# Optimization experiments

Measured on AMD Instinct MI355X. Metric: run time of the kernel, lower is better.

Reference implementation:

```python
import jax, jax.numpy as jnp
import numpy as np

K = 20        # kNN neighborhood size (args.k)
EPS = 1e-5    # BatchNorm eps
SLOPE = 0.2   # LeakyReLU negative slope
B, N = 8, 2048


def lrelu(x):
    return jnp.where(x >= 0, x, SLOPE * x)


def bn_cn(x):  # BatchNorm1d over [B, C, N] (training-mode batch stats, gamma=1, beta=0)
    m = jnp.mean(x, axis=(0, 2), keepdims=True)
    v = jnp.var(x, axis=(0, 2), keepdims=True)
    return (x - m) * jax.lax.rsqrt(v + EPS)


def bn_f(x):  # BatchNorm1d over [B, F]
    m = jnp.mean(x, axis=0, keepdims=True)
    v = jnp.var(x, axis=0, keepdims=True)
    return (x - m) * jax.lax.rsqrt(v + EPS)


def conv_bn(x, w):  # 1x1 Conv1d (no bias) + BN + LeakyReLU; x [B,C,N], w [O,C]
    return lrelu(bn_cn(jnp.einsum('oc,bcn->bon', w, x)))


def knn_idx(x, k):  # x [B,C,N] -> [B,N,k] nearest neighbors, self excluded
    sq = jnp.sum(x * x, axis=1)                                   # [B,N]
    pd = 2.0 * jnp.einsum('bcn,bcm->bnm', x, x) - sq[:, :, None] - sq[:, None, :]
    return jax.lax.top_k(pd, k + 1)[1][:, :, 1:]                  # drop self (max = 0)


def self_att(x, wq, wk, wv, wc):  # SelfAttention block (n_heads=1, scale_dot)
    idx = knn_idx(x, K)                                           # [B,N,K]
    feats = jnp.swapaxes(x, 1, 2)                                 # [B,N,C]
    nb = jax.vmap(lambda f, i: f[i])(feats, idx)                  # [B,N,K,C] gather
    E = wq.shape[0]
    q = feats @ wq.T                                              # [B,N,E]
    kk = nb @ wk.T                                                # [B,N,K,E]
    v = (nb - feats[:, :, None, :]) @ wv.T                        # [B,N,K,V]
    scores = jax.nn.softmax(jnp.einsum('bne,bnke->bnk', q, kk) / np.float32(np.sqrt(E)), axis=-1)
    out = jnp.einsum('bnk,bnkv->bnv', scores, v)                  # [B,N,V]
    res = conv_bn(jnp.swapaxes(out, 1, 2), wc)                    # [B,O,N]
    return jnp.concatenate([res, x], axis=1)


def setup_inputs() -> dict:
    key = jax.random.key(0)
    ks = jax.random.split(key, 32)
    w = lambda k, o, i: jax.random.normal(k, (o, i), jnp.float32) / np.float32(np.sqrt(i))
    d = {'x': jax.random.normal(ks[0], (B, 3, N), jnp.float32)}
    dims = {1: 3, 2: 64, 3: 64, 4: 128}
    j = 1
    for s, c in dims.items():
        for nm in ('wq', 'wk', 'wv', 'wc'):
            d[f'sa{s}_{nm}'] = w(ks[j], c, c); j += 1
    d['conv1_w'] = w(ks[17], 64, 6)
    d['conv2_w'] = w(ks[18], 64, 128)
    d['conv3_w'] = w(ks[19], 128, 128)
    d['conv4_w'] = w(ks[20], 256, 256)
    d['conv5_w'] = w(ks[21], 1024, 512)
    d['lin1_w'] = w(ks[22], 512, 2048); d['lin1_b'] = jnp.zeros((512,), jnp.float32)
    d['lin2_w'] = w(ks[23], 256, 512);  d['lin2_b'] = jnp.zeros((256,), jnp.float32)
    d['lin3_w'] = w(ks[24], 40, 256);   d['lin3_b'] = jnp.zeros((40,), jnp.float32)
    return d


def reference(x, sa1_wq, sa1_wk, sa1_wv, sa1_wc, sa2_wq, sa2_wk, sa2_wv, sa2_wc,
              sa3_wq, sa3_wk, sa3_wv, sa3_wc, sa4_wq, sa4_wk, sa4_wv, sa4_wc,
              conv1_w, conv2_w, conv3_w, conv4_w, conv5_w,
              lin1_w, lin1_b, lin2_w, lin2_b, lin3_w, lin3_b):
    h = self_att(x, sa1_wq, sa1_wk, sa1_wv, sa1_wc)        # [B,6,N]
    x1 = conv_bn(h, conv1_w)                               # [B,64,N]
    h = self_att(x1, sa2_wq, sa2_wk, sa2_wv, sa2_wc)       # [B,128,N]
    x2 = conv_bn(h, conv2_w)                               # [B,64,N]
    h = self_att(x2, sa3_wq, sa3_wk, sa3_wv, sa3_wc)       # [B,128,N]
    x3 = conv_bn(h, conv3_w)                               # [B,128,N]
    h = self_att(x3, sa4_wq, sa4_wk, sa4_wv, sa4_wc)       # [B,256,N]
    x4 = conv_bn(h, conv4_w)                               # [B,256,N]
    xc = jnp.concatenate([x1, x2, x3, x4], axis=1)         # [B,512,N]
    x5 = conv_bn(xc, conv5_w)                              # [B,1024,N]
    p = jnp.concatenate([jnp.max(x5, axis=2), jnp.mean(x5, axis=2)], axis=1)  # [B,2048]
    h = lrelu(bn_f(p @ lin1_w.T + lin1_b))                 # dropout = identity (eval)
    h = lrelu(bn_f(h @ lin2_w.T + lin2_b))
    return h @ lin3_w.T + lin3_b                           # [B,40]
```

## Files before the change

kernel.cpp:

```cpp
#include <hip/hip_runtime.h>
#include <math.h>

#define BB 8
#define NN 2048
#define KNB 20

typedef __attribute__((ext_vector_type(8))) short bf16x8;
typedef __attribute__((ext_vector_type(8))) _Float16 f16x8;
typedef __attribute__((ext_vector_type(4))) float f32x4;

__device__ inline unsigned short f2bf(float f) {
  union { float f; unsigned u; } v; v.f = f;
  unsigned r = v.u + 0x7FFF + ((v.u >> 16) & 1);
  return (unsigned short)(r >> 16);
}

__device__ inline float lrelu(float v) { return v >= 0.f ? v : 0.2f * v; }

template <bool F16SPLIT, bool BF16>
__global__ __launch_bounds__(256) void xprep_kernel(
    const float* __restrict__ in, int inBS, int C,
    float* __restrict__ xT, _Float16* __restrict__ hi, _Float16* __restrict__ lo,
    unsigned short* __restrict__ bf, float* __restrict__ sq) {
  __shared__ float tile[32][33];
  __shared__ float ps[8][33];
  int b = blockIdx.z;
  const float* ip = in + (size_t)b * inBS;
  int c0 = blockIdx.x * 32;
  int r0 = blockIdx.y * 32;
  int tx = threadIdx.x & 31, ty = threadIdx.x >> 5;
  float s = 0.f;
  for (int yy = ty; yy < 32; yy += 8) {
    int r = r0 + yy;
    float v = (r < C) ? ip[(size_t)r * NN + c0 + tx] : 0.f;
    tile[yy][tx] = v;
    s += v * v;
  }
  ps[ty][tx] = s;
  __syncthreads();
  if (ty == 0) {
    float a = ps[0][tx];
#pragma unroll
    for (int u = 1; u < 8; ++u) a += ps[u][tx];
    atomicAdd(&sq[b * NN + c0 + tx], a);
  }
  for (int yy = ty; yy < 32; yy += 8) {
    int c = c0 + yy, r = r0 + tx;
    if (r < C) {
      float v = tile[tx][yy];
      size_t o = (size_t)b * NN * C + (size_t)c * C + r;
      xT[o] = v;
      if (F16SPLIT) {
        _Float16 hv = (_Float16)v;
        hi[o] = hv;
        lo[o] = (_Float16)(v - (float)hv);
      }
      if (BF16) bf[o] = f2bf(v);
    }
  }
}

__global__ __launch_bounds__(256) void xprep3_kernel(const float* __restrict__ in,
                                                     float* __restrict__ xT,
                                                     float* __restrict__ xs4) {
  int b = blockIdx.z;
  int n = blockIdx.x * 256 + threadIdx.x;
  const float* ip = in + (size_t)b * 3 * NN;
  float x0 = ip[n], x1 = ip[NN + n], x2 = ip[2 * NN + n];
  float s = x0 * x0 + x1 * x1 + x2 * x2;
  size_t o = (size_t)b * NN + n;
  xT[o * 3 + 0] = x0; xT[o * 3 + 1] = x1; xT[o * 3 + 2] = x2;
  *(float4*)&xs4[o * 4] = make_float4(x0, x1, x2, s);
}

__global__ __launch_bounds__(256) void prep_mw_kernel(
    const float* __restrict__ wq, const float* __restrict__ wk,
    const float* __restrict__ wv, const float* __restrict__ wc, int C,
    float* __restrict__ M, float* __restrict__ WCV,
    unsigned short* __restrict__ Mb, unsigned short* __restrict__ wcvb, int emitBF) {
  int w = blockIdx.x * 4 + (threadIdx.x >> 6);
  int lane = threadIdx.x & 63;
  int total = 2 * C * C;
  if (w >= total) return;
  float a = 0.f;
  if (w < C * C) {
    int c = w / C, cp = w - c * C;
    for (int e = lane; e < C; e += 64) a += wk[e * C + c] * wq[e * C + cp];
  } else {
    int t = w - C * C;
    int o = t / C, c = t - o * C;
    for (int e = lane; e < C; e += 64) a += wc[o * C + e] * wv[e * C + c];
  }
#pragma unroll
  for (int s = 32; s > 0; s >>= 1) a += __shfl_down(a, s);
  if (lane == 0) {
    if (w < C * C) {
      M[w] = a;
      if (emitBF) Mb[w] = f2bf(a);
    } else {
      int t = w - C * C;
      WCV[t] = a;
      if (emitBF) wcvb[t] = f2bf(a);
    }
  }
}

__global__ __launch_bounds__(256) void convert_bf16_kernel(const float* __restrict__ in,
                                                           unsigned short* __restrict__ out,
                                                           int count) {
  int i = blockIdx.x * 256 + threadIdx.x;
  if (i < count) out[i] = f2bf(in[i]);
}

__global__ __launch_bounds__(256) void transpose_kernel(const float* __restrict__ in, int inBS,
                                                        int R, int Cl, float* __restrict__ out) {
  __shared__ float tile[32][33];
  int b = blockIdx.z;
  const float* ip = in + (size_t)b * inBS;
  float* op = out + (size_t)b * R * Cl;
  int c0 = blockIdx.x * 32, r0 = blockIdx.y * 32;
  int tx = threadIdx.x & 31, ty = threadIdx.x >> 5;
  for (int yy = ty; yy < 32; yy += 8) {
    int r = r0 + yy, c = c0 + tx;
    tile[yy][tx] = (r < R && c < Cl) ? ip[(size_t)r * Cl + c] : 0.f;
  }
  __syncthreads();
  for (int yy = ty; yy < 32; yy += 8) {
    int c = c0 + yy, r = r0 + tx;
    if (c < Cl && r < R) op[(size_t)c * R + r] = tile[tx][yy];
  }
}

__global__ __launch_bounds__(256) void transpose_bf16_kernel(const float* __restrict__ in, int inBS,
                                                             int R, int Cl,
                                                             unsigned short* __restrict__ out) {
  __shared__ float tile[32][33];
  int b = blockIdx.z;
  const float* ip = in + (size_t)b * inBS;
  unsigned short* op = out + (size_t)b * R * Cl;
  int c0 = blockIdx.x * 32, r0 = blockIdx.y * 32;
  int tx = threadIdx.x & 31, ty = threadIdx.x >> 5;
  for (int yy = ty; yy < 32; yy += 8) {
    int r = r0 + yy, c = c0 + tx;
    tile[yy][tx] = (r < R && c < Cl) ? ip[(size_t)r * Cl + c] : 0.f;
  }
  __syncthreads();
  for (int yy = ty; yy < 32; yy += 8) {
    int c = c0 + yy, r = r0 + tx;
    if (c < Cl && r < R) op[(size_t)c * R + r] = f2bf(tile[tx][yy]);
  }
}

template <bool TOUT>
__global__ __launch_bounds__(256, 2) void mfma_gemm_lds_kernel(
    const unsigned short* __restrict__ A, const unsigned short* __restrict__ B,
    float* __restrict__ Z, int O, int K) {
  const int b = blockIdx.z;
  const int n0 = blockIdx.x * 128, o0 = blockIdx.y * 128;
  const int tid = threadIdx.x;
  const int wave = tid >> 6, lane = tid & 63;
  const int wo = wave >> 1, wn = wave & 1;
  const int l16 = lane & 15, q = lane >> 4;
  __shared__ unsigned short Al[2][4096];
  __shared__ unsigned short Bl[2][4096];
  const unsigned short* Ab = A + (size_t)o0 * K;
  const unsigned short* Bb = B + ((size_t)b * NN + n0) * K;

  const int p0 = tid, p1 = tid + 256;
  const int r0 = ((p0 >> 6) << 4) | (p0 & 15), c0 = ((p0 >> 4) & 3) * 8;
  const int r1 = ((p1 >> 6) << 4) | (p1 & 15), c1 = ((p1 >> 4) & 3) * 8;

  bf16x8 ar0, ar1, br0, br1;
  auto gload = [&](int k0) {
    ar0 = *(const bf16x8*)(Ab + (size_t)r0 * K + k0 + c0);
    ar1 = *(const bf16x8*)(Ab + (size_t)r1 * K + k0 + c1);
    br0 = *(const bf16x8*)(Bb + (size_t)r0 * K + k0 + c0);
    br1 = *(const bf16x8*)(Bb + (size_t)r1 * K + k0 + c1);
  };
  auto sstore = [&](int buf) {
    *(bf16x8*)&Al[buf][p0 * 8] = ar0;
    *(bf16x8*)&Al[buf][p1 * 8] = ar1;
    *(bf16x8*)&Bl[buf][p0 * 8] = br0;
    *(bf16x8*)&Bl[buf][p1 * 8] = br1;
  };

  f32x4 acc[4][4];
#pragma unroll
  for (int s = 0; s < 4; ++s)
#pragma unroll
    for (int t = 0; t < 4; ++t) acc[s][t] = (f32x4){0.f, 0.f, 0.f, 0.f};

  gload(0);
  sstore(0);
  int cur = 0;
  for (int k0 = 0; k0 < K; k0 += 32) {
    bool more = (k0 + 32) < K;
    if (more) gload(k0 + 32);
    __syncthreads();
    bf16x8 af[4], bfr[4];
#pragma unroll
    for (int s = 0; s < 4; ++s)
      af[s] = *(const bf16x8*)&Al[cur][((wo * 4 + s) * 64 + q * 16 + l16) * 8];
#pragma unroll
    for (int t = 0; t < 4; ++t)
      bfr[t] = *(const bf16x8*)&Bl[cur][((wn * 4 + t) * 64 + q * 16 + l16) * 8];
#pragma unroll
    for (int s = 0; s < 4; ++s)
#pragma unroll
      for (int t = 0; t < 4; ++t)
        acc[s][t] = __builtin_amdgcn_mfma_f32_16x16x32_bf16(af[s], bfr[t], acc[s][t], 0, 0, 0);
    if (more) sstore(cur ^ 1);
    cur ^= 1;
  }
#pragma unroll
  for (int s = 0; s < 4; ++s)
#pragma unroll
    for (int t = 0; t < 4; ++t) {
      if (TOUT) {
        int n = n0 + wn * 64 + t * 16 + l16;
        int ob = o0 + wo * 64 + s * 16 + q * 4;
        *(f32x4*)&Z[((size_t)b * NN + n) * O + ob] = acc[s][t];
      } else {
        float* zp = Z + ((size_t)b * O + o0 + wo * 64 + s * 16 + q * 4) * NN
                    + n0 + wn * 64 + t * 16 + l16;
#pragma unroll
        for (int r = 0; r < 4; ++r) zp[(size_t)r * NN] = acc[s][t][r];
      }
    }
}

__global__ __launch_bounds__(256, 2) void pd_mfma_kernel(
    const _Float16* __restrict__ xhi, const _Float16* __restrict__ xlo, int C,
    const float* __restrict__ sq, float* __restrict__ P, int b_base) {
  const int bl = blockIdx.z;
  const int b = b_base + bl;
  const int n0 = blockIdx.x * 128, m0 = blockIdx.y * 128;
  const int tid = threadIdx.x;
  const int wave = tid >> 6, lane = tid & 63;
  const int wn_ = wave >> 1, wm_ = wave & 1;
  const int l16 = lane & 15, q = lane >> 4;
  __shared__ _Float16 Ah[4096], Al[4096], Bh[4096], Bl[4096];
  const _Float16* Ahg = xhi + ((size_t)b * NN + n0) * C;
  const _Float16* Alg = xlo + ((size_t)b * NN + n0) * C;
  const _Float16* Bhg = xhi + ((size_t)b * NN + m0) * C;
  const _Float16* Blg = xlo + ((size_t)b * NN + m0) * C;

  const int p0 = tid, p1 = tid + 256;
  const int r0 = ((p0 >> 6) << 4) | (p0 & 15), c0 = ((p0 >> 4) & 3) * 8;
  const int r1 = ((p1 >> 6) << 4) | (p1 & 15), c1 = ((p1 >> 4) & 3) * 8;

  f32x4 acc[4][4];
#pragma unroll
  for (int s = 0; s < 4; ++s)
#pragma unroll
    for (int t = 0; t < 4; ++t) acc[s][t] = (f32x4){0.f, 0.f, 0.f, 0.f};

  for (int k0 = 0; k0 < C; k0 += 32) {
    __syncthreads();
    *(f16x8*)&Ah[p0 * 8] = *(const f16x8*)(Ahg + (size_t)r0 * C + k0 + c0);
    *(f16x8*)&Ah[p1 * 8] = *(const f16x8*)(Ahg + (size_t)r1 * C + k0 + c1);
    *(f16x8*)&Al[p0 * 8] = *(const f16x8*)(Alg + (size_t)r0 * C + k0 + c0);
    *(f16x8*)&Al[p1 * 8] = *(const f16x8*)(Alg + (size_t)r1 * C + k0 + c1);
    *(f16x8*)&Bh[p0 * 8] = *(const f16x8*)(Bhg + (size_t)r0 * C + k0 + c0);
    *(f16x8*)&Bh[p1 * 8] = *(const f16x8*)(Bhg + (size_t)r1 * C + k0 + c1);
    *(f16x8*)&Bl[p0 * 8] = *(const f16x8*)(Blg + (size_t)r0 * C + k0 + c0);
    *(f16x8*)&Bl[p1 * 8] = *(const f16x8*)(Blg + (size_t)r1 * C + k0 + c1);
    __syncthreads();
    f16x8 ah[4], al[4], bh[4], blv[4];
#pragma unroll
    for (int s = 0; s < 4; ++s) {
      int pi = ((wn_ * 4 + s) * 64 + q * 16 + l16) * 8;
      ah[s] = *(const f16x8*)&Ah[pi];
      al[s] = *(const f16x8*)&Al[pi];
    }
#pragma unroll
    for (int t = 0; t < 4; ++t) {
      int pi = ((wm_ * 4 + t) * 64 + q * 16 + l16) * 8;
      bh[t] = *(const f16x8*)&Bh[pi];
      blv[t] = *(const f16x8*)&Bl[pi];
    }
#pragma unroll
    for (int s = 0; s < 4; ++s)
#pragma unroll
      for (int t = 0; t < 4; ++t) {
        acc[s][t] = __builtin_amdgcn_mfma_f32_16x16x32_f16(ah[s], bh[t], acc[s][t], 0, 0, 0);
        acc[s][t] = __builtin_amdgcn_mfma_f32_16x16x32_f16(ah[s], blv[t], acc[s][t], 0, 0, 0);
        acc[s][t] = __builtin_amdgcn_mfma_f32_16x16x32_f16(al[s], bh[t], acc[s][t], 0, 0, 0);
      }
  }
#pragma unroll
  for (int s = 0; s < 4; ++s)
#pragma unroll
    for (int t = 0; t < 4; ++t) {
      int col = m0 + wm_ * 64 + t * 16 + l16;
      float sqv = sq[b * NN + col];
      float* pp = P + ((size_t)bl * NN + n0 + wn_ * 64 + s * 16 + q * 4) * NN + col;
#pragma unroll
      for (int r = 0; r < 4; ++r) pp[(size_t)r * NN] = 2.f * acc[s][t][r] - sqv;
    }
}

__global__ __launch_bounds__(256) void topk_bsort_kernel(const float* __restrict__ P,
                                                         int* __restrict__ idx_out, int b_base) {
  const int wave = threadIdx.x >> 6;
  const int lane = threadIdx.x & 63;
  const int n = blockIdx.x * 4 + wave;
  const int bl = blockIdx.y;
  const int b = b_base + bl;
  const float4* rp = (const float4*)(P + ((size_t)bl * NN + n) * NN);
  unsigned key[32];
#pragma unroll
  for (int q = 0; q < 8; ++q) {
    float4 vv = rp[q * 64 + lane];
    int mb = q * 256 + lane * 4;
    float fv[4] = {vv.x, vv.y, vv.z, vv.w};
#pragma unroll
    for (int j = 0; j < 4; ++j) {
      unsigned u = __float_as_uint(fv[j]);
      unsigned mask = (unsigned)(((int)u) >> 31) | 0x80000000u;
      unsigned sl = (unsigned)(q * 4 + j);
      key[q * 4 + j] = (mb + j == n) ? sl : (((u ^ mask) & 0xFFFFFFE0u) | sl);
    }
  }
#pragma unroll
  for (int k = 2; k <= 32; k <<= 1) {
#pragma unroll
    for (int j = k >> 1; j > 0; j >>= 1) {
#pragma unroll
      for (int i = 0; i < 32; ++i) {
        int l = i ^ j;
        if (l > i) {
          unsigned ka = key[i], kb = key[l];
          unsigned mx = ka > kb ? ka : kb;
          unsigned mn = ka > kb ? kb : ka;
          if ((i & k) == 0) { key[i] = mx; key[l] = mn; }
          else              { key[i] = mn; key[l] = mx; }
        }
      }
    }
  }
  int* op = idx_out + (size_t)(b * NN + n) * KNB;
  for (int k = 0; k < KNB; ++k) {
    unsigned best = key[0];
#pragma unroll
    for (int s = 32; s > 0; s >>= 1) {
      unsigned o = (unsigned)__shfl_xor((int)best, s);
      best = best > o ? best : o;
    }
    unsigned long long bal = __ballot(key[0] == best);
    if (lane == (int)__ffsll(bal) - 1) {
      unsigned sl = key[0] & 31u;
      op[k] = (int)((sl >> 2) * 256u + (unsigned)lane * 4u + (sl & 3u));
#pragma unroll
      for (int j = 0; j < 20; ++j) key[j] = key[j + 1];
    }
  }
}

__global__ __launch_bounds__(256) void topk_c3_kernel(const float* __restrict__ xs4,
                                                      int* __restrict__ idx_out) {
  const int wave = threadIdx.x >> 6;
  const int lane = threadIdx.x & 63;
  const int n = blockIdx.x * 4 + wave;
  const int b = blockIdx.y;
  const float4* xp = (const float4*)(xs4 + (size_t)b * NN * 4);
  float4 me = xp[n];
  float tx = 2.f * me.x, ty = 2.f * me.y, tz = 2.f * me.z;
  unsigned key[32];
#pragma unroll
  for (int s = 0; s < 32; ++s) {
    int m = s * 64 + lane;
    float4 c = xp[m];
    float pd = tx * c.x + ty * c.y + tz * c.z - c.w;
    unsigned u = __float_as_uint(pd);
    unsigned mask = (unsigned)(((int)u) >> 31) | 0x80000000u;
    key[s] = (m == n) ? (unsigned)s : ((((u ^ mask) & 0xFFFFFFE0u)) | (unsigned)s);
  }
#pragma unroll
  for (int k = 2; k <= 32; k <<= 1) {
#pragma unroll
    for (int j = k >> 1; j > 0; j >>= 1) {
#pragma unroll
// ... 207 lines not shown
#pragma unroll
    for (int s = 32; s > 0; s >>= 1) p[k] += __shfl_xor(p[k], s);
  }
  const float scale = (C == 128) ? 0.088388347648318447f : 0.125f;
  float mx = p[0];
#pragma unroll
  for (int k = 1; k < KNB; ++k) mx = fmaxf(mx, p[k]);
  float sum = 0.f;
#pragma unroll
  for (int k = 0; k < KNB; ++k) {
    p[k] = expf((p[k] - mx) * scale);
    sum += p[k];
  }
  float inv = 1.f / sum;
  float a0 = 0.f, a1 = 0.f;
#pragma unroll
  for (int k = 0; k < KNB; ++k) {
    a0 += p[k] * v0[k];
    if (C == 128) a1 += p[k] * v1[k];
  }
  float r0 = a0 * inv - xTb[(size_t)n * C + lane];
  float r1;
  if (C == 128) r1 = a1 * inv - xTb[(size_t)n * C + 64 + lane];
  if (BF16OUT) {
    AGGtb[(size_t)gid * C + lane] = f2bf(r0);
    if (C == 128) AGGtb[(size_t)gid * C + 64 + lane] = f2bf(r1);
  } else {
    AGGt[(size_t)gid * C + lane] = r0;
    if (C == 128) AGGt[(size_t)gid * C + 64 + lane] = r1;
  }
}

template <int C, bool BF16OUT>
__global__ __launch_bounds__(64) void att_wave_kernel(
    const float* __restrict__ xT, const float* __restrict__ UT,
    const int* __restrict__ idx, float* __restrict__ AGGt,
    unsigned short* __restrict__ AGGtb) {
  const int n = blockIdx.x & (NN - 1);
  const int b = blockIdx.x >> 11;
  const int lane = threadIdx.x;
  constexpr int CP = C + 1;
  __shared__ float nb[KNB][CP];
  __shared__ float sl[KNB];
  __shared__ int nidx[KNB];
  __shared__ float ul[C];
  const float* xTb = xT + (size_t)b * NN * C;
  if (lane < KNB) nidx[lane] = idx[(size_t)(b * NN + n) * KNB + lane] & (NN - 1);
  for (int c = lane; c < C; c += 64) ul[c] = UT[((size_t)b * NN + n) * C + c];
  __syncthreads();
  for (int i = lane; i < KNB * C; i += 64) {
    int k = i / C, c = i - k * C;
    nb[k][c] = xTb[(size_t)nidx[k] * C + c];
  }
  __syncthreads();
  float sv = -INFINITY;
  if (lane < KNB) {
    float a = 0.f;
#pragma unroll
    for (int c = 0; c < C; ++c) a += nb[lane][c] * ul[c];
    sv = a / sqrtf((float)C);
  }
  float mx = sv;
#pragma unroll
  for (int s = 32; s > 0; s >>= 1) mx = fmaxf(mx, __shfl_xor(mx, s));
  float e = (lane < KNB) ? expf(sv - mx) : 0.f;
  float sum = e;
#pragma unroll
  for (int s = 32; s > 0; s >>= 1) sum += __shfl_xor(sum, s);
  if (lane < KNB) sl[lane] = e / sum;
  __syncthreads();
  const float* xTn = xTb + (size_t)n * C;
  for (int c = lane; c < C; c += 64) {
    float a = 0.f;
#pragma unroll
    for (int k = 0; k < KNB; ++k) a += sl[k] * nb[k][c];
    float r = a - xTn[c];
    if (BF16OUT)
      AGGtb[((size_t)b * NN + n) * C + c] = f2bf(r);
    else
      AGGt[((size_t)b * NN + n) * C + c] = r;
  }
}

__global__ __launch_bounds__(256) void bn_fused_kernel(const float* __restrict__ z, int O,
                                                       float* __restrict__ out, int outBS, int c0) {
  int o = blockIdx.x;
  int tid = threadIdx.x;
  __shared__ float s1[256], s2[256];
  __shared__ float smv, srv;
  float a1 = 0.f, a2 = 0.f;
  for (int i = tid; i < BB * 512; i += 256) {
    int b = i >> 9, n4 = i & 511;
    float4 v = *(const float4*)&z[((size_t)b * O + o) * NN + n4 * 4];
    a1 += v.x + v.y + v.z + v.w;
    a2 += v.x * v.x + v.y * v.y + v.z * v.z + v.w * v.w;
  }
  s1[tid] = a1; s2[tid] = a2;
  __syncthreads();
  for (int st = 128; st > 0; st >>= 1) {
    if (tid < st) { s1[tid] += s1[tid + st]; s2[tid] += s2[tid + st]; }
    __syncthreads();
  }
  if (tid == 0) {
    float m = s1[0] / (BB * NN);
    float var = s2[0] / (BB * NN) - m * m;
    smv = m; srv = rsqrtf(var + 1e-5f);
  }
  __syncthreads();
  float m = smv, r = srv;
  for (int i = tid; i < BB * 512; i += 256) {
    int b = i >> 9, n4 = i & 511;
    float4 v = *(const float4*)&z[((size_t)b * O + o) * NN + n4 * 4];
    float4 ov;
    ov.x = lrelu((v.x - m) * r); ov.y = lrelu((v.y - m) * r);
    ov.z = lrelu((v.z - m) * r); ov.w = lrelu((v.w - m) * r);
    *(float4*)&out[(size_t)b * outBS + (size_t)(c0 + o) * NN + n4 * 4] = ov;
  }
}

__global__ __launch_bounds__(256) void bn_copy_kernel(const float* __restrict__ z, int O,
                                                      const float* __restrict__ xin, int xbs,
                                                      float* __restrict__ out) {
  int o = blockIdx.x;
  int tid = threadIdx.x;
  int outBS = 2 * O * NN;
  if (o >= O) {
    int c = o - O;
    for (int i = tid; i < BB * 512; i += 256) {
      int b = i >> 9, n4 = i & 511;
      *(float4*)&out[(size_t)b * outBS + (size_t)o * NN + n4 * 4] =
          *(const float4*)&xin[(size_t)b * xbs + (size_t)c * NN + n4 * 4];
    }
    return;
  }
  __shared__ float s1[256], s2[256];
  __shared__ float smv, srv;
  float a1 = 0.f, a2 = 0.f;
  for (int i = tid; i < BB * 512; i += 256) {
    int b = i >> 9, n4 = i & 511;
    float4 v = *(const float4*)&z[((size_t)b * O + o) * NN + n4 * 4];
    a1 += v.x + v.y + v.z + v.w;
    a2 += v.x * v.x + v.y * v.y + v.z * v.z + v.w * v.w;
  }
  s1[tid] = a1; s2[tid] = a2;
  __syncthreads();
  for (int st = 128; st > 0; st >>= 1) {
    if (tid < st) { s1[tid] += s1[tid + st]; s2[tid] += s2[tid + st]; }
    __syncthreads();
  }
  if (tid == 0) {
    float m = s1[0] / (BB * NN);
    float var = s2[0] / (BB * NN) - m * m;
    smv = m; srv = rsqrtf(var + 1e-5f);
  }
  __syncthreads();
  float m = smv, r = srv;
  for (int i = tid; i < BB * 512; i += 256) {
    int b = i >> 9, n4 = i & 511;
    float4 v = *(const float4*)&z[((size_t)b * O + o) * NN + n4 * 4];
    float4 ov;
    ov.x = lrelu((v.x - m) * r); ov.y = lrelu((v.y - m) * r);
    ov.z = lrelu((v.z - m) * r); ov.w = lrelu((v.w - m) * r);
    *(float4*)&out[(size_t)b * outBS + (size_t)o * NN + n4 * 4] = ov;
  }
}

__global__ __launch_bounds__(256) void bn_pool_kernel(const float* __restrict__ z,
                                                      float* __restrict__ p) {
  int o = blockIdx.x;
  int tid = threadIdx.x;
  __shared__ float s1[256], s2[256];
  __shared__ float smv, srv;
  float a1 = 0.f, a2 = 0.f;
  for (int i = tid; i < BB * 512; i += 256) {
    int b = i >> 9, n4 = i & 511;
    float4 v = *(const float4*)&z[((size_t)b * 1024 + o) * NN + n4 * 4];
    a1 += v.x + v.y + v.z + v.w;
    a2 += v.x * v.x + v.y * v.y + v.z * v.z + v.w * v.w;
  }
  s1[tid] = a1; s2[tid] = a2;
  __syncthreads();
  for (int st = 128; st > 0; st >>= 1) {
    if (tid < st) { s1[tid] += s1[tid + st]; s2[tid] += s2[tid + st]; }
    __syncthreads();
  }
  if (tid == 0) {
    float m = s1[0] / (BB * NN);
    float var = s2[0] / (BB * NN) - m * m;
    smv = m; srv = rsqrtf(var + 1e-5f);
  }
  __syncthreads();
  float m = smv, r = srv;
  int b = tid >> 5, l = tid & 31;
  const float* zp = z + ((size_t)b * 1024 + o) * NN;
  float mx = -INFINITY, sm = 0.f;
  for (int j = l; j < 512; j += 32) {
    float4 v = *(const float4*)&zp[j * 4];
    float vx = lrelu((v.x - m) * r), vy = lrelu((v.y - m) * r);
    float vz = lrelu((v.z - m) * r), vw = lrelu((v.w - m) * r);
    mx = fmaxf(mx, fmaxf(fmaxf(vx, vy), fmaxf(vz, vw)));
    sm += vx + vy + vz + vw;
  }
#pragma unroll
  for (int s = 16; s > 0; s >>= 1) {
    mx = fmaxf(mx, __shfl_xor(mx, s));
    sm += __shfl_xor(sm, s);
  }
  if (l == 0) {
    p[b * 2048 + o] = mx;
    p[b * 2048 + 1024 + o] = sm * (1.f / NN);
  }
}

__global__ __launch_bounds__(64) void linear_kernel(const float* __restrict__ in, int IN, int OUT,
                                                    const float* __restrict__ w,
                                                    const float* __restrict__ bias,
                                                    float* __restrict__ out) {
  int o = blockIdx.x;
  int b = o / OUT, f = o % OUT;
  const float* ip = in + (size_t)b * IN;
  const float* wp = w + (size_t)f * IN;
  float a = 0.f;
  for (int i = threadIdx.x; i < IN; i += 64) a += ip[i] * wp[i];
#pragma unroll
  for (int s = 32; s > 0; s >>= 1) a += __shfl_down(a, s);
  if (threadIdx.x == 0) out[o] = a + bias[f];
}

__global__ __launch_bounds__(256) void bnf_kernel(float* __restrict__ t, int F) {
  int f = blockIdx.x * blockDim.x + threadIdx.x;
  if (f >= F) return;
  float s = 0.f, s2 = 0.f;
  for (int b = 0; b < BB; ++b) { float v = t[b * F + f]; s += v; s2 += v * v; }
  float m = s * (1.f / BB);
  float var = s2 * (1.f / BB) - m * m;
  float r = rsqrtf(var + 1e-5f);
  for (int b = 0; b < BB; ++b) {
    float v = (t[b * F + f] - m) * r;
    t[b * F + f] = v >= 0.f ? v : 0.2f * v;
  }
}


struct SAW { const float *wq, *wk, *wv, *wc; };

static inline void run_conv(const float* in, int inBS, int C, int O, const float* w,
                            float* z, hipStream_t st) {
  if (O % 128 == 0)
    conv_gemm128_db_kernel<<<dim3(NN / 128, O / 128, BB), 256, 0, st>>>(in, inBS, C, O, w, z);
  else
    conv_gemm_kernel<false, false><<<dim3(NN / 64, (O + 63) / 64, BB), 256, 0, st>>>(in, inBS, C, O, w, z);
}

template <int C, bool MFMA>
static inline void run_sa(const float* xin, int xbs, SAW w,
                          float* xT, float* UT, float* AGGt, float* z, float* h,
                          float* sq, int* idx,
                          float* M, float* WCV, unsigned short* Mb, unsigned short* wcvb,
                          unsigned short* xTb, unsigned short* AGGtb,
                          _Float16* xhi, _Float16* xlo,
                          float* D, int nbatch, hipStream_t st) {
  static_assert(C % 32 == 0, "run_sa requires C % 32 == 0");
  xprep_kernel<true, MFMA><<<dim3(NN / 32, C / 32, BB), 256, 0, st>>>(
      xin, xbs, C, xT, xhi, xlo, xTb, sq);
  prep_mw_kernel<<<(2 * C * C + 3) / 4, 256, 0, st>>>(w.wq, w.wk, w.wv, w.wc, C,
                                                      M, WCV, Mb, wcvb, MFMA ? 1 : 0);
  for (int bb = 0; bb < BB; bb += nbatch) {
    int nbc = (BB - bb) < nbatch ? (BB - bb) : nbatch;
    pd_mfma_kernel<<<dim3(16, 16, nbc), 256, 0, st>>>(xhi, xlo, C, sq, D, bb);
    topk_bsort_kernel<<<dim3(NN / 4, nbc), 256, 0, st>>>(D, idx, bb);
  }
  if (MFMA) {
    mfma_gemm_lds_kernel<true><<<dim3(NN / 128, C / 128, BB), 256, 0, st>>>(Mb, xTb, UT, C, C);
    att_wave_reg_kernel<C, true><<<BB * NN / 4, 256, 0, st>>>(xT, UT, idx, nullptr, AGGtb);
    mfma_gemm_lds_kernel<false><<<dim3(NN / 128, C / 128, BB), 256, 0, st>>>(wcvb, AGGtb, z, C, C);
  } else {
    conv_gemm_kernel<false, true><<<dim3(NN / 64, C / 64, BB), 256, 0, st>>>(xin, xbs, C, C, M, UT);
    att_wave_reg_kernel<C, false><<<BB * NN / 4, 256, 0, st>>>(xT, UT, idx, AGGt, nullptr);
    conv_gemm_kernel<true, false><<<dim3(NN / 64, C / 64, BB), 256, 0, st>>>(AGGt, NN * C, C, C, WCV, z);
  }
  bn_copy_kernel<<<2 * C, 256, 0, st>>>(z, C, xin, xbs, h);
}

static inline void run_sa3(const float* xin, SAW w,
                           float* xT, float* U, float* UT, float* AGGt, float* AGG,
                           float* z, float* h, float* xs4, int* idx,
                           float* M, float* WCV, unsigned short* Mb, unsigned short* wcvb,
                           hipStream_t st) {
  xprep3_kernel<<<dim3(NN / 256, 1, BB), 256, 0, st>>>(xin, xT, xs4);
  prep_mw_kernel<<<(2 * 3 * 3 + 3) / 4, 256, 0, st>>>(w.wq, w.wk, w.wv, w.wc, 3,
                                                      M, WCV, Mb, wcvb, 0);
  topk_c3_kernel<<<dim3(NN / 4, BB), 256, 0, st>>>(xs4, idx);
  conv_gemm_kernel<false, false><<<dim3(NN / 64, 1, BB), 256, 0, st>>>(xin, 3 * NN, 3, 3, M, U);
  transpose_kernel<<<dim3(NN / 32, 1, BB), 256, 0, st>>>(U, 3 * NN, 3, NN, UT);
  att_wave_kernel<3, false><<<BB * NN, 64, 0, st>>>(xT, UT, idx, AGGt, nullptr);
  transpose_kernel<<<dim3(1, NN / 32, BB), 256, 0, st>>>(AGGt, NN * 3, NN, 3, AGG);
  conv_gemm_kernel<false, false><<<dim3(NN / 64, 1, BB), 256, 0, st>>>(AGG, 3 * NN, 3, 3, WCV, z);
  bn_copy_kernel<<<6, 256, 0, st>>>(z, 3, xin, 3 * NN, h);
}

static inline void run_conv_bn(const float* in, int inBS, int Cin, int O, const float* w,
                               float* z, float* out, int outBS, int c0, hipStream_t st) {
  run_conv(in, inBS, Cin, O, w, z, st);
  bn_fused_kernel<<<O, 256, 0, st>>>(z, O, out, outBS, c0);
}

extern "C" void kernel_launch(void* const* d_in, const int* in_sizes, int n_in,
                              void* d_out, int out_size, void* d_ws, size_t ws_size,
                              hipStream_t stream) {
  const float* x = (const float*)d_in[0];
  SAW sa1{(const float*)d_in[1], (const float*)d_in[2], (const float*)d_in[3], (const float*)d_in[4]};
  SAW sa2{(const float*)d_in[5], (const float*)d_in[6], (const float*)d_in[7], (const float*)d_in[8]};
  SAW sa3{(const float*)d_in[9], (const float*)d_in[10], (const float*)d_in[11], (const float*)d_in[12]};
  SAW sa4{(const float*)d_in[13], (const float*)d_in[14], (const float*)d_in[15], (const float*)d_in[16]};
  const float* conv1_w = (const float*)d_in[17];
  const float* conv2_w = (const float*)d_in[18];
  const float* conv3_w = (const float*)d_in[19];
  const float* conv4_w = (const float*)d_in[20];
  const float* conv5_w = (const float*)d_in[21];
  const float* lin1_w = (const float*)d_in[22];
  const float* lin1_b = (const float*)d_in[23];
  const float* lin2_w = (const float*)d_in[24];
  const float* lin2_b = (const float*)d_in[25];
  const float* lin3_w = (const float*)d_in[26];
  const float* lin3_b = (const float*)d_in[27];

  char* ws = (char*)d_ws;
  size_t off = 0;
  auto take = [&](size_t bytes) -> void* {
    void* p = ws + off;
    off += (bytes + 255) & ~(size_t)255;
    return p;
  };
  float* sqR  = (float*)take((size_t)3 * BB * NN * 4);
  float* xs4  = (float*)take((size_t)BB * NN * 4 * 4);
  int*   idx  = (int*)take((size_t)BB * NN * KNB * 4);
  float* M    = (float*)take((size_t)128 * 128 * 4);
  float* WCV  = (float*)take((size_t)128 * 128 * 4);
  unsigned short* Mb   = (unsigned short*)take((size_t)128 * 128 * 2);
  unsigned short* wcvb = (unsigned short*)take((size_t)128 * 128 * 2);
  unsigned short* w4b  = (unsigned short*)take((size_t)256 * 256 * 2);
  unsigned short* w5b  = (unsigned short*)take((size_t)1024 * 512 * 2);
  float* U    = (float*)take((size_t)BB * 128 * NN * 4);
  float* AGG  = (float*)take((size_t)BB * 128 * NN * 4);
  float* h    = (float*)take((size_t)BB * 256 * NN * 4);
  float* z    = (float*)take((size_t)BB * 1024 * NN * 4);
  float* xc   = (float*)take((size_t)BB * 512 * NN * 4);
  float* p    = (float*)take((size_t)BB * 2048 * 4);
  float* t1   = (float*)take((size_t)BB * 512 * 4);
  float* t2   = (float*)take((size_t)BB * 256 * 4);
  (void)n_in; (void)in_sizes; (void)out_size;

  float* xT = AGG;
  float* AGGt64 = AGG + (size_t)BB * NN * 64;
  float* UT = h;
  float* AGGt1 = z;
  unsigned short* xTb   = (unsigned short*)((char*)h + (size_t)BB * 128 * NN * 4);
  unsigned short* AGGtb = (unsigned short*)((char*)z + (size_t)16 * 1024 * 1024);
  unsigned short* hTb   = (unsigned short*)U;
  unsigned short* xcTb  = (unsigned short*)U;
  _Float16* xhi = (_Float16*)h;
  _Float16* xlo = (_Float16*)((char*)h + (size_t)BB * NN * 128 * 2);

  size_t dfull = (size_t)BB * NN * NN * 4;
  bool fullD = (ws_size > off + dfull + 4096);
  float* D = fullD ? (float*)take(dfull) : z;
  int nbatch = fullD ? BB : 4;

  hipMemsetAsync(sqR, 0, (size_t)3 * BB * NN * 4, stream);

  run_sa3(x, sa1, xT, U, UT, AGGt1, AGG, z, h, xs4, idx, M, WCV, Mb, wcvb, stream);
  run_conv_bn(h, 6 * NN, 6, 64, conv1_w, z, xc, 512 * NN, 0, stream);
  run_sa<64, false>(xc + 0 * NN, 512 * NN, sa2, xT, UT, AGGt64, z, h,
                    sqR + 0 * BB * NN, idx, M, WCV, Mb, wcvb, xTb, AGGtb, xhi, xlo,
                    D, nbatch, stream);
  run_conv_bn(h, 128 * NN, 128, 64, conv2_w, z, xc, 512 * NN, 64, stream);
  run_sa<64, false>(xc + 64 * NN, 512 * NN, sa3, xT, UT, AGGt64, z, h,
                    sqR + 1 * BB * NN, idx, M, WCV, Mb, wcvb, xTb, AGGtb, xhi, xlo,
                    D, nbatch, stream);
  run_conv_bn(h, 128 * NN, 128, 128, conv3_w, z, xc, 512 * NN, 128, stream);
  run_sa<128, true>(xc + 128 * NN, 512 * NN, sa4, xT, UT, nullptr, z, h,
                    sqR + 2 * BB * NN, idx, M, WCV, Mb, wcvb, xTb, AGGtb, xhi, xlo,
                    D, nbatch, stream);
  transpose_bf16_kernel<<<dim3(NN / 32, 8, BB), 256, 0, stream>>>(h, 256 * NN, 256, NN, hTb);
  convert_bf16_kernel<<<(256 * 256 + 255) / 256, 256, 0, stream>>>(conv4_w, w4b, 256 * 256);
  mfma_gemm_lds_kernel<false><<<dim3(NN / 128, 2, BB), 256, 0, stream>>>(w4b, hTb, z, 256, 256);
  bn_fused_kernel<<<256, 256, 0, stream>>>(z, 256, xc, 512 * NN, 256);
  transpose_bf16_kernel<<<dim3(NN / 32, 16, BB), 256, 0, stream>>>(xc, 512 * NN, 512, NN, xcTb);
  convert_bf16_kernel<<<(1024 * 512 + 255) / 256, 256, 0, stream>>>(conv5_w, w5b, 1024 * 512);
  mfma_gemm_lds_kernel<false><<<dim3(NN / 128, 8, BB), 256, 0, stream>>>(w5b, xcTb, z, 1024, 512);
  bn_pool_kernel<<<1024, 256, 0, stream>>>(z, p);
  linear_kernel<<<BB * 512, 64, 0, stream>>>(p, 2048, 512, lin1_w, lin1_b, t1);
  bnf_kernel<<<2, 256, 0, stream>>>(t1, 512);
  linear_kernel<<<BB * 256, 64, 0, stream>>>(t1, 512, 256, lin2_w, lin2_b, t2);
  bnf_kernel<<<1, 256, 0, stream>>>(t2, 256);
  linear_kernel<<<BB * 40, 64, 0, stream>>>(t2, 256, 40, lin3_w, lin3_b, (float*)d_out);
}
```

Measured before the change: 850.7 us.

## Exploit pairwise-distance symmetry, fuse BN stats into GEMM, batch weight prep

The pairwise-distance kernel now computes only upper-triangular 128x128 tiles (136 per batch) and writes each off-diagonal tile's transpose as well, roughly halving the MFMA work for kNN. The conv4/conv5 GEMMs accumulate per-channel sum and sum-of-squares through shuffles, shared-memory atomics and global atomics. This lets the BN kernels skip a full pass over z to compute statistics. All weight-product and bf16 conversion kernels are merged into one up-front launch to cut launch count. In exchange there are extra transposed scattered stores, global atomic contention, and a different floating-point summation order for the BN statistics.

```diff
diff --git a/kernel.cpp b/kernel.cpp
--- a/kernel.cpp
+++ b/kernel.cpp
@@ -73,13 +73,11 @@
   *(float4*)&xs4[o * 4] = make_float4(x0, x1, x2, s);
 }
 
-__global__ __launch_bounds__(256) void prep_mw_kernel(
-    const float* __restrict__ wq, const float* __restrict__ wk,
-    const float* __restrict__ wv, const float* __restrict__ wc, int C,
-    float* __restrict__ M, float* __restrict__ WCV,
-    unsigned short* __restrict__ Mb, unsigned short* __restrict__ wcvb, int emitBF) {
-  int w = blockIdx.x * 4 + (threadIdx.x >> 6);
-  int lane = threadIdx.x & 63;
+__device__ inline void mw_task(const float* __restrict__ wq, const float* __restrict__ wk,
+                               const float* __restrict__ wv, const float* __restrict__ wc,
+                               int C, float* __restrict__ M, float* __restrict__ WCV,
+                               unsigned short* __restrict__ Mb, unsigned short* __restrict__ wcvb,
+                               bool emitBF, int w, int lane) {
   int total = 2 * C * C;
   if (w >= total) return;
   float a = 0.f;
@@ -105,11 +103,48 @@
   }
 }
 
-__global__ __launch_bounds__(256) void convert_bf16_kernel(const float* __restrict__ in,
-                                                           unsigned short* __restrict__ out,
-                                                           int count) {
-  int i = blockIdx.x * 256 + threadIdx.x;
-  if (i < count) out[i] = f2bf(in[i]);
+__global__ __launch_bounds__(256) void weight_prep_kernel(
+    const float* wq1, const float* wk1, const float* wv1, const float* wc1,
+    const float* wq2, const float* wk2, const float* wv2, const float* wc2,
+    const float* wq3, const float* wk3, const float* wv3, const float* wc3,
+    const float* wq4, const float* wk4, const float* wv4, const float* wc4,
+    const float* conv4_w, const float* conv5_w,
+    float* M1, float* W1, float* M2, float* W2, float* M3, float* W3, float* M4, float* W4,
+    unsigned short* Mb4, unsigned short* wcvb4,
+    unsigned short* w4b, unsigned short* w5b) {
+  int bx = blockIdx.x;
+  int lane = threadIdx.x & 63;
+  int wv_ = threadIdx.x >> 6;
+  if (bx < 5) {
+    mw_task(wq1, wk1, wv1, wc1, 3, M1, W1, nullptr, nullptr, false, bx * 4 + wv_, lane);
+    return;
+  }
+  bx -= 5;
+  if (bx < 2048) {
+    mw_task(wq2, wk2, wv2, wc2, 64, M2, W2, nullptr, nullptr, false, bx * 4 + wv_, lane);
+    return;
+  }
+  bx -= 2048;
+  if (bx < 2048) {
+    mw_task(wq3, wk3, wv3, wc3, 64, M3, W3, nullptr, nullptr, false, bx * 4 + wv_, lane);
+    return;
+  }
+  bx -= 2048;
+  if (bx < 8192) {
+    mw_task(wq4, wk4, wv4, wc4, 128, M4, W4, Mb4, wcvb4, true, bx * 4 + wv_, lane);
+    return;
+  }
+  bx -= 8192;
+  if (bx < 256) {
+    int i = bx * 256 + threadIdx.x;
+    w4b[i] = f2bf(conv4_w[i]);
+    return;
+  }
+  bx -= 256;
+  {
+    int i = bx * 256 + threadIdx.x;
+    w5b[i] = f2bf(conv5_w[i]);
+  }
 }
 
 __global__ __launch_bounds__(256) void transpose_kernel(const float* __restrict__ in, int inBS,
@@ -151,10 +186,10 @@
   }
 }
 
-template <bool TOUT>
+template <bool TOUT, bool STATS>
 __global__ __launch_bounds__(256, 2) void mfma_gemm_lds_kernel(
     const unsigned short* __restrict__ A, const unsigned short* __restrict__ B,
-    float* __restrict__ Z, int O, int K) {
+    float* __restrict__ Z, int O, int K, float* __restrict__ gstats) {
   const int b = blockIdx.z;
   const int n0 = blockIdx.x * 128, o0 = blockIdx.y * 128;
   const int tid = threadIdx.x;
@@ -227,14 +262,51 @@
         for (int r = 0; r < 4; ++r) zp[(size_t)r * NN] = acc[s][t][r];
       }
     }
-}
-
-__global__ __launch_bounds__(256, 2) void pd_mfma_kernel(
+  if (STATS) {
+    float psum[16], psq[16];
+#pragma unroll
+    for (int s = 0; s < 4; ++s)
+#pragma unroll
+      for (int r = 0; r < 4; ++r) {
+        float a = 0.f, sa = 0.f;
+#pragma unroll
+        for (int t = 0; t < 4; ++t) { float v = acc[s][t][r]; a += v; sa += v * v; }
+        psum[s * 4 + r] = a; psq[s * 4 + r] = sa;
+      }
+#pragma unroll
+    for (int i = 0; i < 16; ++i) {
+#pragma unroll
+      for (int mm = 1; mm < 16; mm <<= 1) {
+        psum[i] += __shfl_xor(psum[i], mm);
+        psq[i] += __shfl_xor(psq[i], mm);
+      }
+    }
+    __syncthreads();
+    float* sb = (float*)&Al[0][0];
+    sb[tid] = 0.f;
+    __syncthreads();
+    if (l16 == 0) {
+#pragma unroll
+      for (int i = 0; i < 16; ++i) {
+        int ch = wo * 64 + (i >> 2) * 16 + q * 4 + (i & 3);
+        atomicAdd(&sb[ch * 2], psum[i]);
+        atomicAdd(&sb[ch * 2 + 1], psq[i]);
+      }
+    }
+    __syncthreads();
+    atomicAdd(&gstats[o0 * 2 + tid], sb[tid]);
+  }
+}
+
+__global__ __launch_bounds__(256, 2) void pd_mfma_sym_kernel(
     const _Float16* __restrict__ xhi, const _Float16* __restrict__ xlo, int C,
     const float* __restrict__ sq, float* __restrict__ P, int b_base) {
-  const int bl = blockIdx.z;
+  const int bl = blockIdx.y;
   const int b = b_base + bl;
-  const int n0 = blockIdx.x * 128, m0 = blockIdx.y * 128;
+  int ti = 0, xx = blockIdx.x;
+  while (xx >= 16 - ti) { xx -= 16 - ti; ++ti; }
+  const int tj = ti + xx;
+  const int n0 = ti * 128, m0 = tj * 128;
   const int tid = threadIdx.x;
   const int wave = tid >> 6, lane = tid & 63;
   const int wn_ = wave >> 1, wm_ = wave & 1;
@@ -298,6 +370,23 @@
 #pragma unroll
       for (int r = 0; r < 4; ++r) pp[(size_t)r * NN] = 2.f * acc[s][t][r] - sqv;
     }
+  if (ti != tj) {
+#pragma unroll
+    for (int s = 0; s < 4; ++s) {
+      int nb = n0 + wn_ * 64 + s * 16 + q * 4;
+      float4 sqn = *(const float4*)&sq[b * NN + nb];
+#pragma unroll
+      for (int t = 0; t < 4; ++t) {
+        int m = m0 + wm_ * 64 + t * 16 + l16;
+        f32x4 ov;
+        ov[0] = 2.f * acc[s][t][0] - sqn.x;
+        ov[1] = 2.f * acc[s][t][1] - sqn.y;
+        ov[2] = 2.f * acc[s][t][2] - sqn.z;
+        ov[3] = 2.f * acc[s][t][3] - sqn.w;
+        *(f32x4*)&P[((size_t)bl * NN + m) * NN + nb] = ov;
+      }
+    }
+  }
 }
 
 __global__ __launch_bounds__(256) void topk_bsort_kernel(const float* __restrict__ P,
@@ -671,32 +760,42 @@
   }
 }
 
+template <bool PRE>
 __global__ __launch_bounds__(256) void bn_fused_kernel(const float* __restrict__ z, int O,
-                                                       float* __restrict__ out, int outBS, int c0) {
+                                                       float* __restrict__ out, int outBS, int c0,
+                                                       const float* __restrict__ gs) {
   int o = blockIdx.x;
   int tid = threadIdx.x;
-  __shared__ float s1[256], s2[256];
-  __shared__ float smv, srv;
-  float a1 = 0.f, a2 = 0.f;
-  for (int i = tid; i < BB * 512; i += 256) {
-    int b = i >> 9, n4 = i & 511;
-    float4 v = *(const float4*)&z[((size_t)b * O + o) * NN + n4 * 4];
-    a1 += v.x + v.y + v.z + v.w;
-    a2 += v.x * v.x + v.y * v.y + v.z * v.z + v.w * v.w;
-  }
-  s1[tid] = a1; s2[tid] = a2;
-  __syncthreads();
-  for (int st = 128; st > 0; st >>= 1) {
-    if (tid < st) { s1[tid] += s1[tid + st]; s2[tid] += s2[tid + st]; }
-    __syncthreads();
-  }
-  if (tid == 0) {
-    float m = s1[0] / (BB * NN);
-    float var = s2[0] / (BB * NN) - m * m;
-    smv = m; srv = rsqrtf(var + 1e-5f);
-  }
-  __syncthreads();
-  float m = smv, r = srv;
+  float m, r;
+  if (PRE) {
+    float s = gs[o * 2], s2 = gs[o * 2 + 1];
+    m = s / (BB * NN);
+    float var = s2 / (BB * NN) - m * m;
+    r = rsqrtf(var + 1e-5f);
+  } else {
+    __shared__ float s1[256], s2[256];
+    __shared__ float smv, srv;
+    float a1 = 0.f, a2 = 0.f;
+    for (int i = tid; i < BB * 512; i += 256) {
+      int b = i >> 9, n4 = i & 511;
+      float4 v = *(const float4*)&z[((size_t)b * O + o) * NN + n4 * 4];
+      a1 += v.x + v.y + v.z + v.w;
+      a2 += v.x * v.x + v.y * v.y + v.z * v.z + v.w * v.w;
+    }
+    s1[tid] = a1; s2[tid] = a2;
+    __syncthreads();
+    for (int st = 128; st > 0; st >>= 1) {
+      if (tid < st) { s1[tid] += s1[tid + st]; s2[tid] += s2[tid + st]; }
+      __syncthreads();
+    }
+    if (tid == 0) {
+      float mm = s1[0] / (BB * NN);
+      float var = s2[0] / (BB * NN) - mm * mm;
+      smv = mm; srv = rsqrtf(var + 1e-5f);
+    }
+    __syncthreads();
+    m = smv; r = srv;
+  }
   for (int i = tid; i < BB * 512; i += 256) {
     int b = i >> 9, n4 = i & 511;
     float4 v = *(const float4*)&z[((size_t)b * O + o) * NN + n4 * 4];
@@ -754,32 +853,42 @@
   }
 }
 
+template <bool PRE>
 __global__ __launch_bounds__(256) void bn_pool_kernel(const float* __restrict__ z,
-                                                      float* __restrict__ p) {
+                                                      float* __restrict__ p,
+                                                      const float* __restrict__ gs) {
   int o = blockIdx.x;
   int tid = threadIdx.x;
-  __shared__ float s1[256], s2[256];
-  __shared__ float smv, srv;
-  float a1 = 0.f, a2 = 0.f;
-  for (int i = tid; i < BB * 512; i += 256) {
-    int b = i >> 9, n4 = i & 511;
-    float4 v = *(const float4*)&z[((size_t)b * 1024 + o) * NN + n4 * 4];
-    a1 += v.x + v.y + v.z + v.w;
-    a2 += v.x * v.x + v.y * v.y + v.z * v.z + v.w * v.w;
-  }
-  s1[tid] = a1; s2[tid] = a2;
-  __syncthreads();
-  for (int st = 128; st > 0; st >>= 1) {
-    if (tid < st) { s1[tid] += s1[tid + st]; s2[tid] += s2[tid + st]; }
-    __syncthreads();
-  }
-  if (tid == 0) {
-    float m = s1[0] / (BB * NN);
-    float var = s2[0] / (BB * NN) - m * m;
-    smv = m; srv = rsqrtf(var + 1e-5f);
-  }
-  __syncthreads();
-  float m = smv, r = srv;
+  float m, r;
+  if (PRE) {
+    float s = gs[o * 2], s2 = gs[o * 2 + 1];
+    m = s / (BB * NN);
+    float var = s2 / (BB * NN) - m * m;
+    r = rsqrtf(var + 1e-5f);
+  } else {
+    __shared__ float s1[256], s2[256];
+    __shared__ float smv, srv;
+    float a1 = 0.f, a2 = 0.f;
+    for (int i = tid; i < BB * 512; i += 256) {
+      int b = i >> 9, n4 = i & 511;
+      float4 v = *(const float4*)&z[((size_t)b * 1024 + o) * NN + n4 * 4];
+      a1 += v.x + v.y + v.z + v.w;
+      a2 += v.x * v.x + v.y * v.y + v.z * v.z + v.w * v.w;
+    }
+    s1[tid] = a1; s2[tid] = a2;
+    __syncthreads();
+    for (int st = 128; st > 0; st >>= 1) {
+      if (tid < st) { s1[tid] += s1[tid + st]; s2[tid] += s2[tid + st]; }
+      __syncthreads();
+    }
+    if (tid == 0) {
+      float mm = s1[0] / (BB * NN);
+      float var = s2[0] / (BB * NN) - mm * mm;
+      smv = mm; srv = rsqrtf(var + 1e-5f);
+    }
+    __syncthreads();
+    m = smv; r = srv;
+  }
   int b = tid >> 5, l = tid & 31;
   const float* zp = z + ((size_t)b * 1024 + o) * NN;
   float mx = -INFINITY, sm = 0.f;
@@ -842,27 +951,28 @@
 }
 
 template <int C, bool MFMA>
-static inline void run_sa(const float* xin, int xbs, SAW w,
+static inline void run_sa(const float* xin, int xbs,
                           float* xT, float* UT, float* AGGt, float* z, float* h,
                           float* sq, int* idx,
-                          float* M, float* WCV, unsigned short* Mb, unsigned short* wcvb,
+                          const float* M, const float* WCV,
+                          const unsigned short* Mb, const unsigned short* wcvb,
                           unsigned short* xTb, unsigned short* AGGtb,
                           _Float16* xhi, _Float16* xlo,
                           float* D, int nbatch, hipStream_t st) {
   static_assert(C % 32 == 0, "run_sa requires C % 32 == 0");
   xprep_kernel<true, MFMA><<<dim3(NN / 32, C / 32, BB), 256, 0, st>>>(
       xin, xbs, C, xT, xhi, xlo, xTb, sq);
-  prep_mw_kernel<<<(2 * C * C + 3) / 4, 256, 0, st>>>(w.wq, w.wk, w.wv, w.wc, C,
-                                                      M, WCV, Mb, wcvb, MFMA ? 1 : 0);
   for (int bb = 0; bb < BB; bb += nbatch) {
     int nbc = (BB - bb) < nbatch ? (BB - bb) : nbatch;
-    pd_mfma_kernel<<<dim3(16, 16, nbc), 256, 0, st>>>(xhi, xlo, C, sq, D, bb);
+    pd_mfma_sym_kernel<<<dim3(136, nbc), 256, 0, st>>>(xhi, xlo, C, sq, D, bb);
     topk_bsort_kernel<<<dim3(NN / 4, nbc), 256, 0, st>>>(D, idx, bb);
   }
   if (MFMA) {
-    mfma_gemm_lds_kernel<true><<<dim3(NN / 128, C / 128, BB), 256, 0, st>>>(Mb, xTb, UT, C, C);
+    mfma_gemm_lds_kernel<true, false><<<dim3(NN / 128, C / 128, BB), 256, 0, st>>>(
+        (const unsigned short*)Mb, xTb, UT, C, C, nullptr);
     att_wave_reg_kernel<C, true><<<BB * NN / 4, 256, 0, st>>>(xT, UT, idx, nullptr, AGGtb);
-    mfma_gemm_lds_kernel<false><<<dim3(NN / 128, C / 128, BB), 256, 0, st>>>(wcvb, AGGtb, z, C, C);
+    mfma_gemm_lds_kernel<false, false><<<dim3(NN / 128, C / 128, BB), 256, 0, st>>>(
+        (const unsigned short*)wcvb, AGGtb, z, C, C, nullptr);
   } else {
     conv_gemm_kernel<false, true><<<dim3(NN / 64, C / 64, BB), 256, 0, st>>>(xin, xbs, C, C, M, UT);
     att_wave_reg_kernel<C, false><<<BB * NN / 4, 256, 0, st>>>(xT, UT, idx, AGGt, nullptr);
@@ -871,14 +981,11 @@
   bn_copy_kernel<<<2 * C, 256, 0, st>>>(z, C, xin, xbs, h);
 }
 
-static inline void run_sa3(const float* xin, SAW w,
+static inline void run_sa3(const float* xin,
                            float* xT, float* U, float* UT, float* AGGt, float* AGG,
                            float* z, float* h, float* xs4, int* idx,
-                           float* M, float* WCV, unsigned short* Mb, unsigned short* wcvb,
-                           hipStream_t st) {
+                           const float* M, const float* WCV, hipStream_t st) {
   xprep3_kernel<<<dim3(NN / 256, 1, BB), 256, 0, st>>>(xin, xT, xs4);
-  prep_mw_kernel<<<(2 * 3 * 3 + 3) / 4, 256, 0, st>>>(w.wq, w.wk, w.wv, w.wc, 3,
-                                                      M, WCV, Mb, wcvb, 0);
   topk_c3_kernel<<<dim3(NN / 4, BB), 256, 0, st>>>(xs4, idx);
   conv_gemm_kernel<false, false><<<dim3(NN / 64, 1, BB), 256, 0, st>>>(xin, 3 * NN, 3, 3, M, U);
   transpose_kernel<<<dim3(NN / 32, 1, BB), 256, 0, st>>>(U, 3 * NN, 3, NN, UT);
@@ -891,7 +998,7 @@
 static inline void run_conv_bn(const float* in, int inBS, int Cin, int O, const float* w,
                                float* z, float* out, int outBS, int c0, hipStream_t st) {
   run_conv(in, inBS, Cin, O, w, z, st);
-  bn_fused_kernel<<<O, 256, 0, st>>>(z, O, out, outBS, c0);
+  bn_fused_kernel<false><<<O, 256, 0, st>>>(z, O, out, outBS, c0, nullptr);
 }
 
 extern "C" void kernel_launch(void* const* d_in, const int* in_sizes, int n_in,
@@ -922,12 +1029,13 @@
     return p;
   };
   float* sqR  = (float*)take((size_t)3 * BB * NN * 4);
+  float* statsR = (float*)take((size_t)(256 + 1024) * 2 * 4);
   float* xs4  = (float*)take((size_t)BB * NN * 4 * 4);
   int*   idx  = (int*)take((size_t)BB * NN * KNB * 4);
-  float* M    = (float*)take((size_t)128 * 128 * 4);
-  float* WCV  = (float*)take((size_t)128 * 128 * 4);
-  unsigned short* Mb   = (unsigned short*)take((size_t)128 * 128 * 2);
-  unsigned short* wcvb = (unsigned short*)take((size_t)128 * 128 * 2);
+  float* Mall = (float*)take((size_t)4 * 128 * 128 * 4);
+  float* Wall = (float*)take((size_t)4 * 128 * 128 * 4);
+  unsigned short* Mb4   = (unsigned short*)take((size_t)128 * 128 * 2);
+  unsigned short* wcvb4 = (unsigned short*)take((size_t)128 * 128 * 2);
   unsigned short* w4b  = (unsigned short*)take((size_t)256 * 256 * 2);
   unsigned short* w5b  = (unsigned short*)take((size_t)1024 * 512 * 2);
   float* U    = (float*)take((size_t)BB * 128 * NN * 4);
@@ -940,6 +1048,13 @@
   float* t2   = (float*)take((size_t)BB * 256 * 4);
   (void)n_in; (void)in_sizes; (void)out_size;
 
+  float* M1 = Mall + 0 * 16384; float* W1 = Wall + 0 * 16384;
+  float* M2 = Mall + 1 * 16384; float* W2 = Wall + 1 * 16384;
+  float* M3 = Mall + 2 * 16384; float* W3 = Wall + 2 * 16384;
+  float* M4 = Mall + 3 * 16384; float* W4 = Wall + 3 * 16384;
+  float* stats4 = statsR;
+  float* stats5 = statsR + 256 * 2;
+
   float* xT = AGG;
   float* AGGt64 = AGG + (size_t)BB * NN * 64;
   float* UT = h;
@@ -956,29 +1071,33 @@
   float* D = fullD ? (float*)take(dfull) : z;
   int nbatch = fullD ? BB : 4;
 
-  hipMemsetAsync(sqR, 0, (size_t)3 * BB * NN * 4, stream);
-
-  run_sa3(x, sa1, xT, U, UT, AGGt1, AGG, z, h, xs4, idx, M, WCV, Mb, wcvb, stream);
+  hipMemsetAsync(sqR, 0, (size_t)3 * BB * NN * 4 + (size_t)(256 + 1024) * 2 * 4, stream);
+  weight_prep_kernel<<<5 + 2048 + 2048 + 8192 + 256 + 2048, 256, 0, stream>>>(
+      sa1.wq, sa1.wk, sa1.wv, sa1.wc, sa2.wq, sa2.wk, sa2.wv, sa2.wc,
+      sa3.wq, sa3.wk, sa3.wv, sa3.wc, sa4.wq, sa4.wk, sa4.wv, sa4.wc,
+      conv4_w, conv5_w, M1, W1, M2, W2, M3, W3, M4, W4, Mb4, wcvb4, w4b, w5b);
+
+  run_sa3(x, xT, U, UT, AGGt1, AGG, z, h, xs4, idx, M1, W1, stream);
   run_conv_bn(h, 6 * NN, 6, 64, conv1_w, z, xc, 512 * NN, 0, stream);
-  run_sa<64, false>(xc + 0 * NN, 512 * NN, sa2, xT, UT, AGGt64, z, h,
-                    sqR + 0 * BB * NN, idx, M, WCV, Mb, wcvb, xTb, AGGtb, xhi, xlo,
+  run_sa<64, false>(xc + 0 * NN, 512 * NN, xT, UT, AGGt64, z, h,
+                    sqR + 0 * BB * NN, idx, M2, W2, nullptr, nullptr, xTb, AGGtb, xhi, xlo,
                     D, nbatch, stream);
   run_conv_bn(h, 128 * NN, 128, 64, conv2_w, z, xc, 512 * NN, 64, stream);
-  run_sa<64, false>(xc + 64 * NN, 512 * NN, sa3, xT, UT, AGGt64, z, h,
-                    sqR + 1 * BB * NN, idx, M, WCV, Mb, wcvb, xTb, AGGtb, xhi, xlo,
+  run_sa<64, false>(xc + 64 * NN, 512 * NN, xT, UT, AGGt64, z, h,
+                    sqR + 1 * BB * NN, idx, M3, W3, nullptr, nullptr, xTb, AGGtb, xhi, xlo,
                     D, nbatch, stream);
   run_conv_bn(h, 128 * NN, 128, 128, conv3_w, z, xc, 512 * NN, 128, stream);
-  run_sa<128, true>(xc + 128 * NN, 512 * NN, sa4, xT, UT, nullptr, z, h,
-                    sqR + 2 * BB * NN, idx, M, WCV, Mb, wcvb, xTb, AGGtb, xhi, xlo,
+  run_sa<128, true>(xc + 128 * NN, 512 * NN, xT, UT, nullptr, z, h,
+                    sqR + 2 * BB * NN, idx, M4, W4, Mb4, wcvb4, xTb, AGGtb, xhi, xlo,
                     D, nbatch, stream);
   transpose_bf16_kernel<<<dim3(NN / 32, 8, BB), 256, 0, stream>>>(h, 256 * NN, 256, NN, hTb);
-  convert_bf16_kernel<<<(256 * 256 + 255) / 256, 256, 0, stream>>>(conv4_w, w4b, 256 * 256);
-  mfma_gemm_lds_kernel<false><<<dim3(NN / 128, 2, BB), 256, 0, stream>>>(w4b, hTb, z, 256, 256);
-  bn_fused_kernel<<<256, 256, 0, stream>>>(z, 256, xc, 512 * NN, 256);
+  mfma_gemm_lds_kernel<false, true><<<dim3(NN / 128, 2, BB), 256, 0, stream>>>(
+      w4b, hTb, z, 256, 256, stats4);
+  bn_fused_kernel<true><<<256, 256, 0, stream>>>(z, 256, xc, 512 * NN, 256, stats4);
   transpose_bf16_kernel<<<dim3(NN / 32, 16, BB), 256, 0, stream>>>(xc, 512 * NN, 512, NN, xcTb);
-  convert_bf16_kernel<<<(1024 * 512 + 255) / 256, 256, 0, stream>>>(conv5_w, w5b, 1024 * 512);
-  mfma_gemm_lds_kernel<false><<<dim3(NN / 128, 8, BB), 256, 0, stream>>>(w5b, xcTb, z, 1024, 512);
-  bn_pool_kernel<<<1024, 256, 0, stream>>>(z, p);
+  mfma_gemm_lds_kernel<false, true><<<dim3(NN / 128, 8, BB), 256, 0, stream>>>(
+      w5b, xcTb, z, 1024, 512, stats5);
+  bn_pool_kernel<true><<<1024, 256, 0, stream>>>(z, p, stats5);
   linear_kernel<<<BB * 512, 64, 0, stream>>>(p, 2048, 512, lin1_w, lin1_b, t1);
   bnf_kernel<<<2, 256, 0, stream>>>(t1, 512);
   linear_kernel<<<BB * 256, 64, 0, stream>>>(t1, 512, 256, lin2_w, lin2_b, t2);
```

Measured after the change: 850.4 us. About the same (-0.0%).
